# Kernel optimization log

Measured on AMD Instinct MI355X. Metric: run time of the kernel, lower is better.

The kernel has to match this reference:

```python
import jax, jax.numpy as jnp
from jax import lax
import numpy as np

M_RANGE = 2
N_CLASS = 25          # (2*m_range+1)**2 motion classes
IM_CHANNEL = 3        # channels of the last frame


def _conv(x, kernel, m_range):
    # x: [N, n_class, H, W], kernel: [1, n_class, k, k] -> [N, 1, H, W]
    pad = [(m_range, m_range), (m_range, m_range)]
    return lax.conv_general_dilated(
        x, kernel, window_strides=(1, 1), padding=pad,
        dimension_numbers=('NCHW', 'OIHW', 'NCHW'))


def setup_inputs() -> dict:
    key = jax.random.key(0)
    k1, k2, k3 = jax.random.split(key, 3)
    B, H, W = 32, 256, 256
    im_input = jax.random.normal(k1, (B, 2 * IM_CHANNEL, H, W), dtype=jnp.float32)
    m_kernel = jax.random.normal(k2, (1, N_CLASS, 2 * M_RANGE + 1, 2 * M_RANGE + 1), dtype=jnp.float32)
    gt_motion = jax.random.randint(k3, (B, 1, H, W), 0, N_CLASS, dtype=jnp.int32)
    return {'im_input': im_input, 'm_kernel': m_kernel, 'gt_motion': gt_motion}


def reference(im_input, m_kernel, gt_motion):
    B, _, H, W = im_input.shape
    # label2mask: one-hot over motion classes -> [B, n_class, H, W]
    m_mask = jax.nn.one_hot(gt_motion[:, 0], N_CLASS, axis=1, dtype=im_input.dtype)
    # construct_seg: batched conv instead of per-sample loop -> [B, 1, H, W]
    seg = _conv(m_mask, m_kernel, M_RANGE)
    disappear = jax.nn.relu(seg - 1.0)
    appear = jax.nn.relu(1.0 - disappear)
    # construct_image: last im_channel frames, gated by appear
    im = im_input[:, -IM_CHANNEL:] * appear  # appear broadcasts over channel dim
    # per-channel expansion against the motion mask: [B, C, n_class, H, W]
    im_expand = im[:, :, None, :, :] * m_mask[:, None, :, :, :]
    # fold channel dim into batch and run a single batched conv
    pred = _conv(im_expand.reshape(B * IM_CHANNEL, N_CLASS, H, W), m_kernel, M_RANGE)
    pred = pred.reshape(B, IM_CHANNEL, H, W)
    return (pred, m_mask, 1.0 - appear)
```

## Files before the change

### kernel.cpp

```cpp
#include <hip/hip_runtime.h>

#define BB 32
#define H 256
#define W 256
#define NC 25
#define TH 8
#define TW 128
#define GH 16
#define GW 136
#define AH 12
#define AW 132

typedef float f4 __attribute__((ext_vector_type(4)));

__global__ __launch_bounds__(256)
void gtnet_fused(const float* __restrict__ im_input,
                 const float* __restrict__ m_kernel,
                 const int* __restrict__ gt,
                 float* __restrict__ out_pred,
                 float* __restrict__ out_mask,
                 float* __restrict__ out_app)
{
    __shared__ float s_wk[NC * NC];
    __shared__ __align__(16) int    s_gt[GH][GW];
    __shared__ __align__(16) float4 s_img[AH][AW];

    const int tid = threadIdx.x;
    const int bx  = blockIdx.x;
    const int tiles_per_img = (H / TH) * (W / TW);
    const int b  = bx / tiles_per_img;
    const int t  = bx % tiles_per_img;
    const int oh = (t >> 1) * TH;
    const int ow = (t & 1) * TW;

    for (int i = tid; i < NC * NC; i += 256) s_wk[i] = m_kernel[i];

    const int* gtb = gt + b * (H * W);
    for (int i = tid; i < GH * GW; i += 256) {
        int y = i / GW, x = i - y * GW;
        int gy = oh - 4 + y, gx = ow - 4 + x;
        int v = -1;
        if (gy >= 0 && gy < H && gx >= 0 && gx < W) v = gtb[gy * W + gx];
        s_gt[y][x] = v;
    }
    __syncthreads();

    {
        float* mb = out_mask + (size_t)b * (NC * H * W) + (size_t)oh * W + ow;
        const int r  = tid >> 5;
        const int c4 = (tid & 31) * 4;
        const int4 g = *reinterpret_cast<const int4*>(&s_gt[4 + r][4 + c4]);
        const size_t ro = (size_t)r * W + c4;
        #pragma unroll
        for (int c = 0; c < NC; ++c) {
            f4 v;
            v.x = (g.x == c) ? 1.f : 0.f;
            v.y = (g.y == c) ? 1.f : 0.f;
            v.z = (g.z == c) ? 1.f : 0.f;
            v.w = (g.w == c) ? 1.f : 0.f;
            __builtin_nontemporal_store(v, reinterpret_cast<f4*>(&mb[(size_t)c * (H * W) + ro]));
        }
    }

    {
        const float* imb = im_input + ((size_t)b * 6 + 3) * (H * W);
        float* ab = out_app + (size_t)b * (H * W);
        for (int idx = tid; idx < AH * AW; idx += 256) {
            int p = idx / AW, q = idx - p * AW;
            float seg = 0.f;
            #pragma unroll
            for (int i = 0; i < 5; ++i)
                #pragma unroll
                for (int j = 0; j < 5; ++j) {
                    int cls = s_gt[p + i][q + j];
                    seg += (cls >= 0) ? s_wk[cls * NC + i * 5 + j] : 0.f;
                }
            float app = fmaxf(1.f - fmaxf(seg - 1.f, 0.f), 0.f);
            int gy = oh - 2 + p, gx = ow - 2 + q;
            float4 v; v.x = 0.f; v.y = 0.f; v.z = 0.f; v.w = app;
            if (gy >= 0 && gy < H && gx >= 0 && gx < W) {
                int o = gy * W + gx;
                v.x = imb[o] * app;
                v.y = imb[H * W + o] * app;
                v.z = imb[2 * H * W + o] * app;
            }
            s_img[p][q] = v;
            if (p >= 2 && p < 2 + TH && q >= 2 && q < 2 + TW)
                __builtin_nontemporal_store(1.f - app,
                    &ab[(size_t)(oh + p - 2) * W + (ow + q - 2)]);
        }
    }
    __syncthreads();

    {
        const int x0 = tid & 127;
        const int y0 = (tid >> 7) * 4;
        float acc[4][3];
        #pragma unroll
        for (int dy = 0; dy < 4; ++dy) {
            acc[dy][0] = 0.f; acc[dy][1] = 0.f; acc[dy][2] = 0.f;
        }

        #pragma unroll
        for (int sy = 0; sy < 8; ++sy) {
            #pragma unroll
            for (int sx = 0; sx < 5; ++sx) {
                const int p = y0 + sy, q = x0 + sx;
                const float4 im4 = s_img[p][q];
                const int cls = s_gt[p + 2][q + 2];
                const int cw  = (cls >= 0) ? cls * NC : 0;
                #pragma unroll
                for (int dy = 0; dy < 4; ++dy) {
                    const int i = sy - dy;
                    if (i < 0 || i > 4) continue;
                    const float w = s_wk[cw + i * 5 + sx];
                    acc[dy][0] += im4.x * w;
                    acc[dy][1] += im4.y * w;
                    acc[dy][2] += im4.z * w;
                }
            }
        }

        float* pb = out_pred + (size_t)b * 3 * H * W;
        #pragma unroll
        for (int ch = 0; ch < 3; ++ch)
            #pragma unroll
            for (int dy = 0; dy < 4; ++dy)
                __builtin_nontemporal_store(acc[dy][ch],
                    &pb[(size_t)(ch * H + oh + y0 + dy) * W + ow + x0]);
    }
}

extern "C" void kernel_launch(void* const* d_in, const int* in_sizes, int n_in,
                              void* d_out, int out_size, void* d_ws, size_t ws_size,
                              hipStream_t stream) {
    const float* im_input = (const float*)d_in[0];
    const float* m_kernel = (const float*)d_in[1];
    const int*   gt       = (const int*)d_in[2];

    float* out_pred = (float*)d_out;
    float* out_mask = out_pred + (size_t)BB * 3 * H * W;
    float* out_app  = out_mask + (size_t)BB * NC * H * W;

    const int blocks = BB * (H / TH) * (W / TW);
    gtnet_fused<<<blocks, 256, 0, stream>>>(im_input, m_kernel, gt,
                                            out_pred, out_mask, out_app);
}
```

Before: 319.2 us.

## Split one-hot mask writing into a separate streaming kernel

Moves the one-hot mask output out of the fused tile kernel into a dedicated kernel where each thread reads four labels straight from global memory and writes 25 class planes. The pred/appear kernel no longer carries the large mask store traffic. The cost is a second launch, a second read of the labels, and no overlap between the mask stores and the convolution work, since both kernels run serially on one stream.

```diff
diff --git a/kernel.cpp b/kernel.cpp
--- a/kernel.cpp
+++ b/kernel.cpp
@@ -14,12 +14,34 @@
 typedef float f4 __attribute__((ext_vector_type(4)));
 
 __global__ __launch_bounds__(256)
-void gtnet_fused(const float* __restrict__ im_input,
-                 const float* __restrict__ m_kernel,
-                 const int* __restrict__ gt,
-                 float* __restrict__ out_pred,
-                 float* __restrict__ out_mask,
-                 float* __restrict__ out_app)
+void gtnet_mask(const int* __restrict__ gt, float* __restrict__ out_mask)
+{
+    const int g     = blockIdx.x * 256 + threadIdx.x;
+    const int lane4 = g & 63;
+    const int rowg  = g >> 6;
+    const int b     = rowg >> 8;
+    const int row   = rowg & 255;
+
+    const int4 gv = *reinterpret_cast<const int4*>(&gt[(b * H + row) * W + lane4 * 4]);
+    float* mb = out_mask + (size_t)b * (NC * H * W) + (size_t)row * W + lane4 * 4;
+
+    #pragma unroll
+    for (int c = 0; c < NC; ++c) {
+        f4 v;
+        v.x = (gv.x == c) ? 1.f : 0.f;
+        v.y = (gv.y == c) ? 1.f : 0.f;
+        v.z = (gv.z == c) ? 1.f : 0.f;
+        v.w = (gv.w == c) ? 1.f : 0.f;
+        __builtin_nontemporal_store(v, reinterpret_cast<f4*>(&mb[(size_t)c * (H * W)]));
+    }
+}
+
+__global__ __launch_bounds__(256)
+void gtnet_pred(const float* __restrict__ im_input,
+                const float* __restrict__ m_kernel,
+                const int* __restrict__ gt,
+                float* __restrict__ out_pred,
+                float* __restrict__ out_app)
 {
     __shared__ float s_wk[NC * NC];
     __shared__ __align__(16) int    s_gt[GH][GW];
@@ -44,23 +66,6 @@
         s_gt[y][x] = v;
     }
     __syncthreads();
-
-    {
-        float* mb = out_mask + (size_t)b * (NC * H * W) + (size_t)oh * W + ow;
-        const int r  = tid >> 5;
-        const int c4 = (tid & 31) * 4;
-        const int4 g = *reinterpret_cast<const int4*>(&s_gt[4 + r][4 + c4]);
-        const size_t ro = (size_t)r * W + c4;
-        #pragma unroll
-        for (int c = 0; c < NC; ++c) {
-            f4 v;
-            v.x = (g.x == c) ? 1.f : 0.f;
-            v.y = (g.y == c) ? 1.f : 0.f;
-            v.z = (g.z == c) ? 1.f : 0.f;
-            v.w = (g.w == c) ? 1.f : 0.f;
-            __builtin_nontemporal_store(v, reinterpret_cast<f4*>(&mb[(size_t)c * (H * W) + ro]));
-        }
-    }
 
     {
         const float* imb = im_input + ((size_t)b * 6 + 3) * (H * W);
@@ -142,7 +147,8 @@
     float* out_mask = out_pred + (size_t)BB * 3 * H * W;
     float* out_app  = out_mask + (size_t)BB * NC * H * W;
 
-    const int blocks = BB * (H / TH) * (W / TW);
-    gtnet_fused<<<blocks, 256, 0, stream>>>(im_input, m_kernel, gt,
-                                            out_pred, out_mask, out_app);
+    gtnet_mask<<<BB * H / 4, 256, 0, stream>>>(gt, out_mask);
+    const int blocksB = BB * (H / TH) * (W / TW);
+    gtnet_pred<<<blocksB, 256, 0, stream>>>(im_input, m_kernel, gt,
+                                            out_pred, out_app);
 }
```

New measurement: 323.2 us. About the same (+1.2%).
